# Optimization experiments

Measured on AMD Instinct MI355X. Metric: run time of the kernel, lower is better.

Reference implementation:

```python
import jax, jax.numpy as jnp
import numpy as np

PATCH = 16  # conv kernel size == stride


def _patch_embed(im, W, b):
    # im: (B, C, H, W) NCHW; W: (hidden, C, s, s); returns (B, h, w, hidden)
    out = jax.lax.conv_general_dilated(
        im, W, window_strides=(PATCH, PATCH), padding='VALID',
        dimension_numbers=('NCHW', 'OIHW', 'NCHW'))
    out = out + b[None, :, None, None]
    return jnp.transpose(out, (0, 2, 3, 1))  # (B, h, w, hidden)


def setup_inputs() -> dict:
    key = jax.random.key(0)
    k1, k2, k3, k4 = jax.random.split(key, 4)
    B, C, H, Wd = 64, 3, 224, 224
    hidden = 384
    x = jax.random.normal(k1, (B, C, H, Wd), dtype=jnp.float32)
    y = jax.random.normal(k2, (B, C, H, Wd), dtype=jnp.float32)
    fan_in = C * PATCH * PATCH
    bound = 1.0 / np.sqrt(fan_in)
    W = jax.random.uniform(k3, (hidden, C, PATCH, PATCH), dtype=jnp.float32,
                           minval=-bound, maxval=bound)
    b = jax.random.uniform(k4, (hidden,), dtype=jnp.float32,
                           minval=-bound, maxval=bound)
    return {'x': x, 'y': y, 'W': W, 'b': b}


def reference(x, y, W, b):
    B = x.shape[0]
    xp = _patch_embed(x, W, b)  # (B, h, w, C)
    yp = _patch_embed(y, W, b)  # (B, h, w, C)
    h, w = xp.shape[1], xp.shape[2]
    logp = jax.nn.log_softmax(xp, axis=-1)          # (B, h, w, C)
    q = jax.lax.stop_gradient(jax.nn.softmax(yp, axis=-1))  # detached targets
    # CE[i, j] = mean over (h, w) of -(q_j * logp_i).sum(-1)
    # Faithful factorization of the (B, B, h, w, C) broadcast in the original.
    CE = -jnp.einsum('ihwc,jhwc->ij', logp, q) / (h * w)  # (B, B)
    close = jnp.trace(CE) / B
    far = (CE.sum() - jnp.trace(CE)) / (B * B - B)
    return close / far
```

## Files before the change

### kernel.cpp

```cpp
#include <hip/hip_runtime.h>

#define HID   384
#define K_PE  768
#define IMGST 150528
#define POS   196

typedef unsigned short ushort_t;
using f32x4  = __attribute__((ext_vector_type(4))) float;
using short8 = __attribute__((ext_vector_type(8))) short;

__device__ __forceinline__ unsigned bfpack(float lo, float hi) {
    union { float f; unsigned u; } a, b; a.f = lo; b.f = hi;
    unsigned ra = (a.u + 0x7fffu + ((a.u >> 16) & 1u)) >> 16;
    unsigned rb = (b.u + 0x7fffu + ((b.u >> 16) & 1u)) & 0xffff0000u;
    return ra | rb;
}
__device__ __forceinline__ unsigned cvtpk(float lo, float hi) {
    unsigned r;
    asm("v_cvt_pk_bf16_f32 %0, %1, %2" : "=v"(r) : "v"(lo), "v"(hi));
    return r;
}
__device__ __forceinline__ float bf2f(unsigned hibits) {
    union { unsigned u; float f; } v; v.u = hibits; return v.f;
}

__global__ __launch_bounds__(256) void prep(const float* __restrict__ W,
                                            ushort_t* __restrict__ Wfrag,
                                            float* __restrict__ scal) {
    const int t = blockIdx.x * 256 + threadIdx.x;
    if (t < 4) scal[t] = 0.f;
    const int n  = t / 96;
    const int ko = t - n * 96;
    const float4 a  = *(const float4*)(W + (size_t)n * K_PE + ko * 8);
    const float4 bb = *(const float4*)(W + (size_t)n * K_PE + ko * 8 + 4);
    uint4 pq;
    pq.x = bfpack(a.x, a.y);   pq.y = bfpack(a.z, a.w);
    pq.z = bfpack(bb.x, bb.y); pq.w = bfpack(bb.z, bb.w);
    const int nt    = n >> 4;
    const int kc    = ko >> 2;
    const int lanew = (ko & 3) * 16 + (n & 15);
    ((uint4*)Wfrag)[(nt * 24 + kc) * 64 + lanew] = pq;
}

__global__ __launch_bounds__(256, 2) void pef(
    const float* __restrict__ x, const float* __restrict__ y,
    const ushort_t* __restrict__ Wfrag, const float* __restrict__ bias,
    float* __restrict__ scal, unsigned* __restrict__ Zg) {
    const int blk = blockIdx.x;
    const int pi  = blk >> 5;
    const int ig  = blk & 31;

    __shared__ __align__(16) ushort_t As[2][8 * 456];
    __shared__ float Smx[4][32], Ssx[4][32], Smy[4][32], Ssy[4][32];
    __shared__ float sT[4];

    const int tid  = threadIdx.x;
    const int wave = tid >> 6;
    const int lane = tid & 63;
    const int lm   = lane & 15;
    const int lq   = lane >> 4;

    const int rr   = tid >> 5;
    const int sj   = tid & 31;
    const int st   = rr >> 2;
    const int simg = (rr >> 1) & 1;
    const int skh  = rr & 1;
    const int sq   = sj & 1;
    const int spj  = sj >> 1;
    const bool sact = sj < 28;
    const float* srow = (st ? y : x) +
        (size_t)(ig * 2 + simg) * IMGST + pi * 3584 + skh * 224 + sj * 8;
    const int ainner = st * 224 + simg * 112 + spj * 8;
    const int aoff0  = (skh * 2 + sq) * 456 + ainner;
    const int aoff1  = ((skh + 2) * 2 + sq) * 456 + ainner;

    int ard[2][2];
#pragma unroll
    for (int t = 0; t < 2; ++t)
#pragma unroll
        for (int mi = 0; mi < 2; ++mi) {
            int m = mi * 16 + lm; if (m > 27) m = 27;
            const int img = (m >= 14) ? 1 : 0;
            const int pj  = m - img * 14;
            ard[t][mi] = t * 224 + img * 112 + pj * 8;
        }
    const int ob0 = lq * 456, ob1 = (4 + lq) * 456;

    f32x4 accx[2][6] = {};
    f32x4 accy[2][6] = {};

#define LOADB(B, KC)                                                          \
    {                                                                         \
        _Pragma("unroll")                                                     \
        for (int ni = 0; ni < 6; ++ni)                                        \
            B[ni] = *(const short8*)(Wfrag +                                  \
                    ((size_t)((wave * 6 + ni) * 24 + (KC)) * 64 + lane) * 8); \
    }
#define MFMA24(AF, B, ACX, ACY)                                               \
    {                                                                         \
        _Pragma("unroll")                                                     \
        for (int mi = 0; mi < 2; ++mi)                                        \
            _Pragma("unroll")                                                 \
            for (int ni = 0; ni < 6; ++ni) {                                  \
                ACX[mi][ni] = __builtin_amdgcn_mfma_f32_16x16x32_bf16(        \
                    AF[0][mi], B[ni], ACX[mi][ni], 0, 0, 0);                  \
                ACY[mi][ni] = __builtin_amdgcn_mfma_f32_16x16x32_bf16(        \
                    AF[1][mi], B[ni], ACY[mi][ni], 0, 0, 0);                  \
            }                                                                 \
    }

    if (sact) {
        const float4 f0 = *(const float4*)(srow);
        const float4 f1 = *(const float4*)(srow + 4);
        const float4 f2 = *(const float4*)(srow + 448);
        const float4 f3 = *(const float4*)(srow + 452);
        uint4 p0, p1;
        p0.x = bfpack(f0.x, f0.y); p0.y = bfpack(f0.z, f0.w);
        p0.z = bfpack(f1.x, f1.y); p0.w = bfpack(f1.z, f1.w);
        p1.x = bfpack(f2.x, f2.y); p1.y = bfpack(f2.z, f2.w);
        p1.z = bfpack(f3.x, f3.y); p1.w = bfpack(f3.z, f3.w);
        *(uint4*)&As[0][aoff0] = p0;
        *(uint4*)&As[0][aoff1] = p1;
    }
    short8 b0[6], b1[6], bn[6];
    LOADB(b0, 0)
    __syncthreads();

#pragma unroll 2
    for (int kk = 0; kk < 12; ++kk) {
        const int cur = kk & 1;
        const bool have = sact && (kk < 11);
        const int nb = ((kk + 1) >> 2) * 50176 + ((kk + 1) & 3) * 896;
        float4 f0{}, f1{}, f2{}, f3{};
        if (have) {
            f0 = *(const float4*)(srow + nb);
            f1 = *(const float4*)(srow + nb + 4);
            f2 = *(const float4*)(srow + nb + 448);
            f3 = *(const float4*)(srow + nb + 452);
        }
        LOADB(b1, kk * 2 + 1)
        short8 af[2][2];
#pragma unroll
        for (int t = 0; t < 2; ++t)
#pragma unroll
            for (int mi = 0; mi < 2; ++mi)
                af[t][mi] = *(const short8*)&As[cur][ob0 + ard[t][mi]];
        MFMA24(af, b0, accx, accy)
        const int kn2 = (kk < 11) ? (kk + 1) * 2 : 0;
        LOADB(bn, kn2)
#pragma unroll
        for (int t = 0; t < 2; ++t)
#pragma unroll
            for (int mi = 0; mi < 2; ++mi)
                af[t][mi] = *(const short8*)&As[cur][ob1 + ard[t][mi]];
        MFMA24(af, b1, accx, accy)
        if (have) {
            uint4 p0, p1;
            p0.x = bfpack(f0.x, f0.y); p0.y = bfpack(f0.z, f0.w);
            p0.z = bfpack(f1.x, f1.y); p0.w = bfpack(f1.z, f1.w);
            p1.x = bfpack(f2.x, f2.y); p1.y = bfpack(f2.z, f2.w);
            p1.z = bfpack(f3.x, f3.y); p1.w = bfpack(f3.z, f3.w);
            *(uint4*)&As[cur ^ 1][aoff0] = p0;
            *(uint4*)&As[cur ^ 1][aoff1] = p1;
        }
#pragma unroll
        for (int ni = 0; ni < 6; ++ni) b0[ni] = bn[ni];
        __syncthreads();
    }
#undef LOADB
#undef MFMA24

#pragma unroll
    for (int ni = 0; ni < 6; ++ni) {
        const float bv = bias[wave * 96 + ni * 16 + lm];
#pragma unroll
        for (int mi = 0; mi < 2; ++mi)
#pragma unroll
            for (int r = 0; r < 4; ++r) {
                accx[mi][ni][r] += bv;
                accy[mi][ni][r] += bv;
            }
    }

    float mx[2][4], my_[2][4];
#pragma unroll
    for (int mi = 0; mi < 2; ++mi)
#pragma unroll
        for (int r = 0; r < 4; ++r) {
            float a = accx[mi][0][r], bb = accy[mi][0][r];
#pragma unroll
            for (int ni = 1; ni < 6; ++ni) {
                a  = fmaxf(a,  accx[mi][ni][r]);
                bb = fmaxf(bb, accy[mi][ni][r]);
            }
            mx[mi][r] = a; my_[mi][r] = bb;
        }
#pragma unroll
    for (int off = 1; off < 16; off <<= 1)
#pragma unroll
        for (int mi = 0; mi < 2; ++mi)
#pragma unroll
            for (int r = 0; r < 4; ++r) {
                mx[mi][r]  = fmaxf(mx[mi][r],  __shfl_xor(mx[mi][r],  off));
                my_[mi][r] = fmaxf(my_[mi][r], __shfl_xor(my_[mi][r], off));
            }
    if (lm == 0)
#pragma unroll
        for (int mi = 0; mi < 2; ++mi)
#pragma unroll
            for (int r = 0; r < 4; ++r) {
                Smx[wave][mi * 16 + lq * 4 + r] = mx[mi][r];
                Smy[wave][mi * 16 + lq * 4 + r] = my_[mi][r];
            }
    __syncthreads();
#pragma unroll
    for (int mi = 0; mi < 2; ++mi)
#pragma unroll
        for (int r = 0; r < 4; ++r) {
            const int row = mi * 16 + lq * 4 + r;
            mx[mi][r]  = fmaxf(fmaxf(Smx[0][row], Smx[1][row]),
                               fmaxf(Smx[2][row], Smx[3][row]));
            my_[mi][r] = fmaxf(fmaxf(Smy[0][row], Smy[1][row]),
                               fmaxf(Smy[2][row], Smy[3][row]));
        }

    float sx[2][4], sy[2][4];
#pragma unroll
    for (int mi = 0; mi < 2; ++mi)
#pragma unroll
        for (int r = 0; r < 4; ++r) {
            float a = 0.f, bb = 0.f;
#pragma unroll
            for (int ni = 0; ni < 6; ++ni) {
                a  += __expf(accx[mi][ni][r] - mx[mi][r]);
                bb += __expf(accy[mi][ni][r] - my_[mi][r]);
            }
            sx[mi][r] = a; sy[mi][r] = bb;
        }
#pragma unroll
    for (int off = 1; off < 16; off <<= 1)
#pragma unroll
        for (int mi = 0; mi < 2; ++mi)
#pragma unroll
            for (int r = 0; r < 4; ++r) {
                sx[mi][r] += __shfl_xor(sx[mi][r], off);
                sy[mi][r] += __shfl_xor(sy[mi][r], off);
            }
    if (lm == 0)
#pragma unroll
        for (int mi = 0; mi < 2; ++mi)
#pragma unroll
            for (int r = 0; r < 4; ++r) {
                Ssx[wave][mi * 16 + lq * 4 + r] = sx[mi][r];
                Ssy[wave][mi * 16 + lq * 4 + r] = sy[mi][r];
            }
    __syncthreads();
    float shx[2][4], invy[2][4];
#pragma unroll
    for (int mi = 0; mi < 2; ++mi)
#pragma unroll
        for (int r = 0; r < 4; ++r) {
            const int row = mi * 16 + lq * 4 + r;
            const float ssx = Ssx[0][row] + Ssx[1][row] + Ssx[2][row] + Ssx[3][row];
            const float ssy = Ssy[0][row] + Ssy[1][row] + Ssy[2][row] + Ssy[3][row];
            shx[mi][r]  = mx[mi][r] + __logf(ssx);
            invy[mi][r] = 1.f / ssy;
        }

    float T = 0.f;
#pragma unroll
    for (int mi = 0; mi < 2; ++mi)
#pragma unroll
        for (int r = 0; r < 4; ++r) {
            const int m = mi * 16 + lq * 4 + r;
            if (m < 28) {
                const int img = (m >= 14) ? 1 : 0;
                const int pj  = m - img * 14;
                const size_t lb = ((size_t)(pi * 14 + pj) * 64 + ig * 2 + img) * 384
                                  + wave * 96 + lm;
                const float sh  = shx[mi][r];
                const float mm  = my_[mi][r];
                const float inv = invy[mi][r];
#pragma unroll
                for (int ni = 0; ni < 6; ++ni) {
                    const float lp = accx[mi][ni][r] - sh;
                    const float qv = __expf(accy[mi][ni][r] - mm) * inv;
                    T += lp * qv;
                    Zg[lb + ni * 16] = cvtpk(lp, qv);
                }
            }
        }
#pragma unroll
    for (int off = 32; off > 0; off >>= 1) T += __shfl_xor(T, off);
    if (lane == 0) sT[wave] = T;
    __syncthreads();
    if (tid == 0) atomicAdd(&scal[0], sT[0] + sT[1] + sT[2] + sT[3]);
}

__global__ __launch_bounds__(768) void fin(const unsigned* __restrict__ Zg,
                                           float* __restrict__ scal,
                                           float* __restrict__ out) {
    const int p = blockIdx.x;
    const int t = threadIdx.x;
    const int h = t / 384;
    const int c = t - h * 384;
    float L = 0.f, Q = 0.f;
#pragma unroll 4
    for (int i = 0; i < 32; ++i) {
        const unsigned u = Zg[((size_t)p * 64 + h * 32 + i) * 384 + c];
        L += bf2f(u << 16);
        Q += bf2f(u & 0xffff0000u);
    }
    __shared__ float LL[384], QQ[384];
    if (h == 0) { LL[c] = L; QQ[c] = Q; }
    __syncthreads();
    float s = 0.f;
    if (h == 1) s = (LL[c] + L) * (QQ[c] + Q);
#pragma unroll
    for (int off = 32; off > 0; off >>= 1) s += __shfl_xor(s, off);
    __shared__ float sw[12];
    if ((t & 63) == 0) sw[t >> 6] = s;
    __syncthreads();
    if (t == 0) {
        float Sp = 0.f;
#pragma unroll
        for (int w = 0; w < 12; ++w) Sp += sw[w];
        atomicAdd(&scal[1], Sp);
        __threadfence();
        const int old = atomicAdd((int*)&scal[3], 1);
        if (old == POS - 1) {
            const float T = atomicAdd(&scal[0], 0.f);
            const float S = atomicAdd(&scal[1], 0.f);
            out[0] = 63.f * T / (S - T);
        }
    }
}

extern "C" void kernel_launch(void* const* d_in, const int* in_sizes, int n_in,
                              void* d_out, int out_size, void* d_ws, size_t ws_size,
                              hipStream_t stream) {
    const float* x = (const float*)d_in[0];
    const float* y = (const float*)d_in[1];
    const float* W = (const float*)d_in[2];
    const float* b = (const float*)d_in[3];
    float* out = (float*)d_out;

    char* ws = (char*)d_ws;
    float*    scal  = (float*)ws;
    ushort_t* Wfrag = (ushort_t*)(ws + 1024);
    unsigned* Zg    = (unsigned*)(ws + 590848);

    prep<<<144, 256, 0, stream>>>(W, Wfrag, scal);
    pef<<<448, 256, 0, stream>>>(x, y, Wfrag, b, scal, Zg);
    fin<<<196, 768, 0, stream>>>(Zg, scal, out);
}
```

Before: 136.6 us.

## Halve per-block M tile to one image per block, doubling grid

Each patch-embed block now handles one image's 14 patches instead of two images' 28. The M tile drops from 32 to 16 rows, so accumulators, LDS staging and launch bounds shrink and the grid doubles to 896 blocks. The aim is more waves per CU and better latency hiding and load balance. In exchange, each block reuses the weight fragments over half as many rows, so weight traffic per MFMA doubles, and 2 of the 16 MFMA rows are wasted padding.

```diff
diff --git a/kernel.cpp b/kernel.cpp
--- a/kernel.cpp
+++ b/kernel.cpp
@@ -42,16 +42,16 @@
     ((uint4*)Wfrag)[(nt * 24 + kc) * 64 + lanew] = pq;
 }
 
-__global__ __launch_bounds__(256, 2) void pef(
+__global__ __launch_bounds__(256, 4) void pef(
     const float* __restrict__ x, const float* __restrict__ y,
     const ushort_t* __restrict__ Wfrag, const float* __restrict__ bias,
     float* __restrict__ scal, unsigned* __restrict__ Zg) {
     const int blk = blockIdx.x;
-    const int pi  = blk >> 5;
-    const int ig  = blk & 31;
-
-    __shared__ __align__(16) ushort_t As[2][8 * 456];
-    __shared__ float Smx[4][32], Ssx[4][32], Smy[4][32], Ssy[4][32];
+    const int pi  = blk >> 6;
+    const int img = blk & 63;
+
+    __shared__ __align__(16) ushort_t As[2][8 * 228];
+    __shared__ float Smx[4][16], Ssx[4][16], Smy[4][16], Ssy[4][16];
     __shared__ float sT[4];
 
     const int tid  = threadIdx.x;
@@ -63,31 +63,23 @@
     const int rr   = tid >> 5;
     const int sj   = tid & 31;
     const int st   = rr >> 2;
-    const int simg = (rr >> 1) & 1;
-    const int skh  = rr & 1;
+    const int skh  = rr & 3;
     const int sq   = sj & 1;
     const int spj  = sj >> 1;
     const bool sact = sj < 28;
     const float* srow = (st ? y : x) +
-        (size_t)(ig * 2 + simg) * IMGST + pi * 3584 + skh * 224 + sj * 8;
-    const int ainner = st * 224 + simg * 112 + spj * 8;
-    const int aoff0  = (skh * 2 + sq) * 456 + ainner;
-    const int aoff1  = ((skh + 2) * 2 + sq) * 456 + ainner;
-
-    int ard[2][2];
-#pragma unroll
-    for (int t = 0; t < 2; ++t)
-#pragma unroll
-        for (int mi = 0; mi < 2; ++mi) {
-            int m = mi * 16 + lm; if (m > 27) m = 27;
-            const int img = (m >= 14) ? 1 : 0;
-            const int pj  = m - img * 14;
-            ard[t][mi] = t * 224 + img * 112 + pj * 8;
-        }
-    const int ob0 = lq * 456, ob1 = (4 + lq) * 456;
-
-    f32x4 accx[2][6] = {};
-    f32x4 accy[2][6] = {};
+        (size_t)img * IMGST + pi * 3584 + skh * 224 + sj * 8;
+    const int aoff = (skh * 2 + sq) * 228 + st * 112 + spj * 8;
+
+    int ard[2];
+    {
+        int m = lm; if (m > 13) m = 13;
+        ard[0] = m * 8;
+        ard[1] = 112 + m * 8;
+    }
+
+    f32x4 accx[6] = {};
+    f32x4 accy[6] = {};
 
 #define LOADB(B, KC)                                                          \
     {                                                                         \
@@ -96,200 +88,159 @@
             B[ni] = *(const short8*)(Wfrag +                                  \
                     ((size_t)((wave * 6 + ni) * 24 + (KC)) * 64 + lane) * 8); \
     }
-#define MFMA24(AF, B, ACX, ACY)                                               \
+#define MFMA12(AFX, AFY, B)                                                   \
     {                                                                         \
         _Pragma("unroll")                                                     \
-        for (int mi = 0; mi < 2; ++mi)                                        \
-            _Pragma("unroll")                                                 \
-            for (int ni = 0; ni < 6; ++ni) {                                  \
-                ACX[mi][ni] = __builtin_amdgcn_mfma_f32_16x16x32_bf16(        \
-                    AF[0][mi], B[ni], ACX[mi][ni], 0, 0, 0);                  \
-                ACY[mi][ni] = __builtin_amdgcn_mfma_f32_16x16x32_bf16(        \
-                    AF[1][mi], B[ni], ACY[mi][ni], 0, 0, 0);                  \
-            }                                                                 \
-    }
-
+        for (int ni = 0; ni < 6; ++ni) {                                      \
+            accx[ni] = __builtin_amdgcn_mfma_f32_16x16x32_bf16(               \
+                AFX, B[ni], accx[ni], 0, 0, 0);                               \
+            accy[ni] = __builtin_amdgcn_mfma_f32_16x16x32_bf16(               \
+                AFY, B[ni], accy[ni], 0, 0, 0);                               \
+        }                                                                     \
+    }
+
+    short8 b0[6], b1[6], bn[6];
+    LOADB(b0, 0)
     if (sact) {
         const float4 f0 = *(const float4*)(srow);
         const float4 f1 = *(const float4*)(srow + 4);
-        const float4 f2 = *(const float4*)(srow + 448);
-        const float4 f3 = *(const float4*)(srow + 452);
-        uint4 p0, p1;
+        uint4 p0;
         p0.x = bfpack(f0.x, f0.y); p0.y = bfpack(f0.z, f0.w);
         p0.z = bfpack(f1.x, f1.y); p0.w = bfpack(f1.z, f1.w);
-        p1.x = bfpack(f2.x, f2.y); p1.y = bfpack(f2.z, f2.w);
-        p1.z = bfpack(f3.x, f3.y); p1.w = bfpack(f3.z, f3.w);
-        *(uint4*)&As[0][aoff0] = p0;
-        *(uint4*)&As[0][aoff1] = p1;
-    }
-    short8 b0[6], b1[6], bn[6];
-    LOADB(b0, 0)
+        *(uint4*)&As[0][aoff] = p0;
+    }
     __syncthreads();
 
 #pragma unroll 2
     for (int kk = 0; kk < 12; ++kk) {
         const int cur = kk & 1;
+        LOADB(b1, kk * 2 + 1)
+        float4 f0{}, f1{};
         const bool have = sact && (kk < 11);
-        const int nb = ((kk + 1) >> 2) * 50176 + ((kk + 1) & 3) * 896;
-        float4 f0{}, f1{}, f2{}, f3{};
         if (have) {
+            const int nb = ((kk + 1) >> 2) * 50176 + ((kk + 1) & 3) * 896;
             f0 = *(const float4*)(srow + nb);
             f1 = *(const float4*)(srow + nb + 4);
-            f2 = *(const float4*)(srow + nb + 448);
-            f3 = *(const float4*)(srow + nb + 452);
-        }
-        LOADB(b1, kk * 2 + 1)
-        short8 af[2][2];
-#pragma unroll
-        for (int t = 0; t < 2; ++t)
-#pragma unroll
-            for (int mi = 0; mi < 2; ++mi)
-                af[t][mi] = *(const short8*)&As[cur][ob0 + ard[t][mi]];
-        MFMA24(af, b0, accx, accy)
+        }
+        short8 afx = *(const short8*)&As[cur][lq * 228 + ard[0]];
+        short8 afy = *(const short8*)&As[cur][lq * 228 + ard[1]];
+        MFMA12(afx, afy, b0)
         const int kn2 = (kk < 11) ? (kk + 1) * 2 : 0;
         LOADB(bn, kn2)
-#pragma unroll
-        for (int t = 0; t < 2; ++t)
-#pragma unroll
-            for (int mi = 0; mi < 2; ++mi)
-                af[t][mi] = *(const short8*)&As[cur][ob1 + ard[t][mi]];
-        MFMA24(af, b1, accx, accy)
+        afx = *(const short8*)&As[cur][(4 + lq) * 228 + ard[0]];
+        afy = *(const short8*)&As[cur][(4 + lq) * 228 + ard[1]];
+        MFMA12(afx, afy, b1)
         if (have) {
-            uint4 p0, p1;
+            uint4 p0;
             p0.x = bfpack(f0.x, f0.y); p0.y = bfpack(f0.z, f0.w);
             p0.z = bfpack(f1.x, f1.y); p0.w = bfpack(f1.z, f1.w);
-            p1.x = bfpack(f2.x, f2.y); p1.y = bfpack(f2.z, f2.w);
-            p1.z = bfpack(f3.x, f3.y); p1.w = bfpack(f3.z, f3.w);
-            *(uint4*)&As[cur ^ 1][aoff0] = p0;
-            *(uint4*)&As[cur ^ 1][aoff1] = p1;
+            *(uint4*)&As[cur ^ 1][aoff] = p0;
         }
 #pragma unroll
         for (int ni = 0; ni < 6; ++ni) b0[ni] = bn[ni];
         __syncthreads();
     }
 #undef LOADB
-#undef MFMA24
+#undef MFMA12
 
 #pragma unroll
     for (int ni = 0; ni < 6; ++ni) {
         const float bv = bias[wave * 96 + ni * 16 + lm];
 #pragma unroll
-        for (int mi = 0; mi < 2; ++mi)
-#pragma unroll
-            for (int r = 0; r < 4; ++r) {
-                accx[mi][ni][r] += bv;
-                accy[mi][ni][r] += bv;
+        for (int r = 0; r < 4; ++r) {
+            accx[ni][r] += bv;
+            accy[ni][r] += bv;
+        }
+    }
+
+    float mx[4], my_[4];
+#pragma unroll
+    for (int r = 0; r < 4; ++r) {
+        float a = accx[0][r], bb = accy[0][r];
+#pragma unroll
+        for (int ni = 1; ni < 6; ++ni) {
+            a  = fmaxf(a,  accx[ni][r]);
+            bb = fmaxf(bb, accy[ni][r]);
+        }
+        mx[r] = a; my_[r] = bb;
+    }
+#pragma unroll
+    for (int off = 1; off < 16; off <<= 1)
+#pragma unroll
+        for (int r = 0; r < 4; ++r) {
+            mx[r]  = fmaxf(mx[r],  __shfl_xor(mx[r],  off));
+            my_[r] = fmaxf(my_[r], __shfl_xor(my_[r], off));
+        }
+    if (lm == 0)
+#pragma unroll
+        for (int r = 0; r < 4; ++r) {
+            Smx[wave][lq * 4 + r] = mx[r];
+            Smy[wave][lq * 4 + r] = my_[r];
+        }
+    __syncthreads();
+#pragma unroll
+    for (int r = 0; r < 4; ++r) {
+        const int row = lq * 4 + r;
+        mx[r]  = fmaxf(fmaxf(Smx[0][row], Smx[1][row]),
+                       fmaxf(Smx[2][row], Smx[3][row]));
+        my_[r] = fmaxf(fmaxf(Smy[0][row], Smy[1][row]),
+                       fmaxf(Smy[2][row], Smy[3][row]));
+    }
+
+    float sx[4], sy[4];
+#pragma unroll
+    for (int r = 0; r < 4; ++r) {
+        float a = 0.f, bb = 0.f;
+#pragma unroll
+        for (int ni = 0; ni < 6; ++ni) {
+            a  += __expf(accx[ni][r] - mx[r]);
+            bb += __expf(accy[ni][r] - my_[r]);
+        }
+        sx[r] = a; sy[r] = bb;
+    }
+#pragma unroll
+    for (int off = 1; off < 16; off <<= 1)
+#pragma unroll
+        for (int r = 0; r < 4; ++r) {
+            sx[r] += __shfl_xor(sx[r], off);
+            sy[r] += __shfl_xor(sy[r], off);
+        }
+    if (lm == 0)
+#pragma unroll
+        for (int r = 0; r < 4; ++r) {
+            Ssx[wave][lq * 4 + r] = sx[r];
+            Ssy[wave][lq * 4 + r] = sy[r];
+        }
+    __syncthreads();
+    float shx[4], invy[4];
+#pragma unroll
+    for (int r = 0; r < 4; ++r) {
+        const int row = lq * 4 + r;
+        const float ssx = Ssx[0][row] + Ssx[1][row] + Ssx[2][row] + Ssx[3][row];
+        const float ssy = Ssy[0][row] + Ssy[1][row] + Ssy[2][row] + Ssy[3][row];
+        shx[r]  = mx[r] + __logf(ssx);
+        invy[r] = 1.f / ssy;
+    }
+
+    float T = 0.f;
+#pragma unroll
+    for (int r = 0; r < 4; ++r) {
+        const int m = lq * 4 + r;
+        if (m < 14) {
+            const size_t lb = ((size_t)(pi * 14 + m) * 64 + img) * 384
+                              + wave * 96 + lm;
+            const float sh  = shx[r];
+            const float mm  = my_[r];
+            const float inv = invy[r];
+#pragma unroll
+            for (int ni = 0; ni < 6; ++ni) {
+                const float lp = accx[ni][r] - sh;
+                const float qv = __expf(accy[ni][r] - mm) * inv;
+                T += lp * qv;
+                Zg[lb + ni * 16] = cvtpk(lp, qv);
             }
-    }
-
-    float mx[2][4], my_[2][4];
-#pragma unroll
-    for (int mi = 0; mi < 2; ++mi)
-#pragma unroll
-        for (int r = 0; r < 4; ++r) {
-            float a = accx[mi][0][r], bb = accy[mi][0][r];
-#pragma unroll
-            for (int ni = 1; ni < 6; ++ni) {
-                a  = fmaxf(a,  accx[mi][ni][r]);
-                bb = fmaxf(bb, accy[mi][ni][r]);
-            }
-            mx[mi][r] = a; my_[mi][r] = bb;
-        }
-#pragma unroll
-    for (int off = 1; off < 16; off <<= 1)
-#pragma unroll
-        for (int mi = 0; mi < 2; ++mi)
-#pragma unroll
-            for (int r = 0; r < 4; ++r) {
-                mx[mi][r]  = fmaxf(mx[mi][r],  __shfl_xor(mx[mi][r],  off));
-                my_[mi][r] = fmaxf(my_[mi][r], __shfl_xor(my_[mi][r], off));
-            }
-    if (lm == 0)
-#pragma unroll
-        for (int mi = 0; mi < 2; ++mi)
-#pragma unroll
-            for (int r = 0; r < 4; ++r) {
-                Smx[wave][mi * 16 + lq * 4 + r] = mx[mi][r];
-                Smy[wave][mi * 16 + lq * 4 + r] = my_[mi][r];
-            }
-    __syncthreads();
-#pragma unroll
-    for (int mi = 0; mi < 2; ++mi)
-#pragma unroll
-        for (int r = 0; r < 4; ++r) {
-            const int row = mi * 16 + lq * 4 + r;
-            mx[mi][r]  = fmaxf(fmaxf(Smx[0][row], Smx[1][row]),
-                               fmaxf(Smx[2][row], Smx[3][row]));
-            my_[mi][r] = fmaxf(fmaxf(Smy[0][row], Smy[1][row]),
-                               fmaxf(Smy[2][row], Smy[3][row]));
-        }
-
-    float sx[2][4], sy[2][4];
-#pragma unroll
-    for (int mi = 0; mi < 2; ++mi)
-#pragma unroll
-        for (int r = 0; r < 4; ++r) {
-            float a = 0.f, bb = 0.f;
-#pragma unroll
-            for (int ni = 0; ni < 6; ++ni) {
-                a  += __expf(accx[mi][ni][r] - mx[mi][r]);
-                bb += __expf(accy[mi][ni][r] - my_[mi][r]);
-            }
-            sx[mi][r] = a; sy[mi][r] = bb;
-        }
-#pragma unroll
-    for (int off = 1; off < 16; off <<= 1)
-#pragma unroll
-        for (int mi = 0; mi < 2; ++mi)
-#pragma unroll
-            for (int r = 0; r < 4; ++r) {
-                sx[mi][r] += __shfl_xor(sx[mi][r], off);
-                sy[mi][r] += __shfl_xor(sy[mi][r], off);
-            }
-    if (lm == 0)
-#pragma unroll
-        for (int mi = 0; mi < 2; ++mi)
-#pragma unroll
-            for (int r = 0; r < 4; ++r) {
-                Ssx[wave][mi * 16 + lq * 4 + r] = sx[mi][r];
-                Ssy[wave][mi * 16 + lq * 4 + r] = sy[mi][r];
-            }
-    __syncthreads();
-    float shx[2][4], invy[2][4];
-#pragma unroll
-    for (int mi = 0; mi < 2; ++mi)
-#pragma unroll
-        for (int r = 0; r < 4; ++r) {
-            const int row = mi * 16 + lq * 4 + r;
-            const float ssx = Ssx[0][row] + Ssx[1][row] + Ssx[2][row] + Ssx[3][row];
-            const float ssy = Ssy[0][row] + Ssy[1][row] + Ssy[2][row] + Ssy[3][row];
-            shx[mi][r]  = mx[mi][r] + __logf(ssx);
-            invy[mi][r] = 1.f / ssy;
-        }
-
-    float T = 0.f;
-#pragma unroll
-    for (int mi = 0; mi < 2; ++mi)
-#pragma unroll
-        for (int r = 0; r < 4; ++r) {
-            const int m = mi * 16 + lq * 4 + r;
-            if (m < 28) {
-                const int img = (m >= 14) ? 1 : 0;
-                const int pj  = m - img * 14;
-                const size_t lb = ((size_t)(pi * 14 + pj) * 64 + ig * 2 + img) * 384
-                                  + wave * 96 + lm;
-                const float sh  = shx[mi][r];
-                const float mm  = my_[mi][r];
-                const float inv = invy[mi][r];
-#pragma unroll
-                for (int ni = 0; ni < 6; ++ni) {
-                    const float lp = accx[mi][ni][r] - sh;
-                    const float qv = __expf(accy[mi][ni][r] - mm) * inv;
-                    T += lp * qv;
-                    Zg[lb + ni * 16] = cvtpk(lp, qv);
-                }
-            }
-        }
+        }
+    }
 #pragma unroll
     for (int off = 32; off > 0; off >>= 1) T += __shfl_xor(T, off);
     if (lane == 0) sT[wave] = T;
@@ -351,6 +302,6 @@
     unsigned* Zg    = (unsigned*)(ws + 590848);
 
     prep<<<144, 256, 0, stream>>>(W, Wfrag, scal);
-    pef<<<448, 256, 0, stream>>>(x, y, Wfrag, b, scal, Zg);
+    pef<<<896, 256, 0, stream>>>(x, y, Wfrag, b, scal, Zg);
     fin<<<196, 768, 0, stream>>>(Zg, scal, out);
 }
```

Measured after the change: 171.6 us. 25.6% more time.
